# Kernel tuning notes

Hardware: AMD Instinct MI355X
Metric: run time of the kernel (lower is better)

## Reference

```python
import jax, jax.numpy as jnp
import numpy as np
from jax import lax

# Shared Conv2d [1,1] + BN + ReLU is represented as a per-point affine (BN folded
# into conv weight/bias at eval) followed by ReLU, matching inference-mode math.

B, N1, N2, K = 8, 8192, 2048, 8
C1, C2 = 64, 128
MLP0, MLP1, MLP2 = 128, 128, 128  # mlp=[128,128], mlp2=[128]


def setup_inputs() -> dict:
    key = jax.random.key(0)
    ks = jax.random.split(key, 10)
    sc = lambda fan_in: 1.0 / np.sqrt(fan_in)
    return {
        "xyz1": jax.random.normal(ks[0], (B, N1, 3), jnp.float32),
        "xyz2": jax.random.normal(ks[1], (B, N2, 3), jnp.float32),
        "feat1": jax.random.normal(ks[2], (B, N1, C1), jnp.float32),
        "feat2": jax.random.normal(ks[3], (B, N2, C2), jnp.float32),
        "W0": jax.random.normal(ks[4], (C2 + 3, MLP0), jnp.float32) * sc(C2 + 3),
        "b0": jnp.zeros((MLP0,), jnp.float32),
        "W1": jax.random.normal(ks[5], (MLP0, MLP1), jnp.float32) * sc(MLP0),
        "b1": jnp.zeros((MLP1,), jnp.float32),
        "W2": jax.random.normal(ks[6], (MLP1 + C1, MLP2), jnp.float32) * sc(MLP1 + C1),
        "b2": jnp.zeros((MLP2,), jnp.float32),
    }


def _knn_idx(xyz1, xyz2, k):
    # squared distances (B, N1, N2); top-k nearest in xyz2 for each xyz1 point
    d2 = jnp.sum((xyz1[:, :, None, :] - xyz2[:, None, :, :]) ** 2, axis=-1)
    _, idx = lax.top_k(-d2, k)  # (B, N1, K)
    return idx


def _gather(src, idx):
    # src: (B, N2, C), idx: (B, N1, K) -> (B, N1, K, C)
    return jax.vmap(lambda s, i: s[i])(src, idx)


def reference(xyz1, xyz2, feat1, feat2, W0, b0, W1, b1, W2, b2):
    idx = _knn_idx(xyz1, xyz2, K)
    xyz2_g = _gather(xyz2, idx)            # (B, N1, K, 3)
    feat2_g = _gather(feat2, idx)          # (B, N1, K, C2)
    xyz_diff = xyz2_g - xyz1[:, :, None, :]
    net = jnp.concatenate([feat2_g, xyz_diff], axis=-1)  # (B, N1, K, C2+3)
    net = jax.nn.relu(net @ W0 + b0)
    net = jax.nn.relu(net @ W1 + b1)       # (B, N1, K, MLP1)
    pooled = jnp.max(net, axis=2)          # max pooling over neighbors
    cat = jnp.concatenate([pooled, feat1], axis=-1)      # (B, N1, MLP1+C1)
    out = jax.nn.relu(cat @ W2 + b2)       # (B, N1, MLP2)
    return out
```

## Files before the change

kernel.cpp:

```cpp
#include <hip/hip_runtime.h>
#include <hip/hip_bf16.h>

constexpr int B_  = 8;
constexpr int N1_ = 8192;
constexpr int N2_ = 2048;
constexpr int K_  = 8;

typedef short bf16x8 __attribute__((ext_vector_type(8)));
typedef float f32x4  __attribute__((ext_vector_type(4)));

__device__ __forceinline__ short f2b(float x) {
    __hip_bfloat16 h = __float2bfloat16(x);
    return *reinterpret_cast<short*>(&h);
}

#define CASF(a, b) { const float _lo = fminf(a, b); \
                     const float _hi = fmaxf(a, b); \
                     (a) = _lo; (b) = _hi; }

__global__ __launch_bounds__(256) void prep_feat2(const float* __restrict__ feat2,
                                                  short* __restrict__ feat2b) {
    const int i = blockIdx.x * 256 + threadIdx.x;
    const float4 v = ((const float4*)feat2)[i];
    uint2 o;
    o.x = (unsigned short)f2b(v.x) | ((unsigned)(unsigned short)f2b(v.y) << 16);
    o.y = (unsigned short)f2b(v.z) | ((unsigned)(unsigned short)f2b(v.w) << 16);
    ((uint2*)feat2b)[i] = o;
}

__global__ __launch_bounds__(256) void prep_weights(
    const float* __restrict__ W0, const float* __restrict__ W1,
    const float* __restrict__ W2, const float* __restrict__ xyz2,
    short* __restrict__ W0T, short* __restrict__ W1T, short* __restrict__ W2T,
    float4* __restrict__ xpack) {
    int i = blockIdx.x * 256 + threadIdx.x;
    if (i < 128 * 160) {
        const int n = i / 160, k = i % 160;
        W0T[i] = (k < 131) ? f2b(W0[k * 128 + n]) : (short)0;
        return;
    }
    i -= 128 * 160;
    if (i < 128 * 128) {
        const int n = i >> 7, k = i & 127;
        W1T[i] = f2b(W1[k * 128 + n]);
        return;
    }
    i -= 128 * 128;
    if (i < 128 * 192) {
        const int n = i / 192, k = i % 192;
        W2T[i] = f2b(W2[k * 128 + n]);
        return;
    }
    i -= 128 * 192;
    xpack[i] = make_float4(xyz2[i * 3 + 0], xyz2[i * 3 + 1], xyz2[i * 3 + 2], 0.f);
}

constexpr int LCAP = 76;

__global__ __launch_bounds__(256) void knn_lazy(const float* __restrict__ xyz1,
                                                const float4* __restrict__ xpack,
                                                int* __restrict__ idx) {
    __shared__ __align__(16) unsigned short sMem[78 * 256];
    float* sD = (float*)sMem;
    int*   sI = (int*)sMem + 64 * 33;

    const int b = blockIdx.y;
    const int lane = threadIdx.x & 63;
    const int s = threadIdx.x >> 6;
    const int tid = threadIdx.x;
    const int n = blockIdx.x * 64 + lane;

    const float* q = xyz1 + ((size_t)b * N1_ + n) * 3;
    const float qx = q[0], qy = q[1], qz = q[2];
    const float4* P = xpack + (size_t)b * N2_ + s * 512;

    float bd[K_];
#pragma unroll
    for (int t = 0; t < K_; ++t) bd[t] = 3.0e38f;
    int cnt = 0;

    for (int j0 = 0; j0 < 512; j0 += 8) {
        float xf[8];
#pragma unroll
        for (int u = 0; u < 8; ++u) {
#pragma clang fp contract(off)
            const float4 p = P[j0 + u];
            const float dx = qx - p.x;
            const float dy = qy - p.y;
            const float dz = qz - p.z;
            const float dx2 = dx * dx;
            const float dy2 = dy * dy;
            const float dz2 = dz * dz;
            xf[u] = (dx2 + dy2) + dz2;
        }
        const float thr = bd[K_ - 1];
#pragma unroll
        for (int u = 0; u < 8; ++u) {
            const bool acc = xf[u] < thr;
            if (acc) {
                const int capped = cnt < LCAP ? cnt : LCAP;
                sMem[capped * 256 + tid] = (unsigned short)(j0 + u);
                cnt++;
            }
        }
        CASF(xf[0], xf[1]); CASF(xf[2], xf[3]); CASF(xf[4], xf[5]); CASF(xf[6], xf[7]);
        CASF(xf[0], xf[2]); CASF(xf[1], xf[3]); CASF(xf[4], xf[6]); CASF(xf[5], xf[7]);
        CASF(xf[1], xf[2]); CASF(xf[5], xf[6]); CASF(xf[0], xf[4]); CASF(xf[3], xf[7]);
        CASF(xf[1], xf[5]); CASF(xf[2], xf[6]);
        CASF(xf[1], xf[4]); CASF(xf[3], xf[6]);
        CASF(xf[2], xf[4]); CASF(xf[3], xf[5]);
        CASF(xf[3], xf[4]);
        float t0 = fminf(bd[0], xf[7]);
        float t1 = fminf(bd[1], xf[6]);
        float t2 = fminf(bd[2], xf[5]);
        float t3 = fminf(bd[3], xf[4]);
        float t4 = fminf(bd[4], xf[3]);
        float t5 = fminf(bd[5], xf[2]);
        float t6 = fminf(bd[6], xf[1]);
        float t7 = fminf(bd[7], xf[0]);
        CASF(t0, t4); CASF(t1, t5); CASF(t2, t6); CASF(t3, t7);
        CASF(t0, t2); CASF(t1, t3); CASF(t4, t6); CASF(t5, t7);
        CASF(t0, t1); CASF(t2, t3); CASF(t4, t5); CASF(t6, t7);
        bd[0] = t0; bd[1] = t1; bd[2] = t2; bd[3] = t3;
        bd[4] = t4; bd[5] = t5; bd[6] = t6; bd[7] = t7;
    }

    float rd[K_];
    int   ri[K_];
#pragma unroll
    for (int t = 0; t < K_; ++t) { rd[t] = 3.0e38f; ri[t] = 0; }
    const int m = cnt < LCAP ? cnt : LCAP;
    for (int t = 0;; ++t) {
        const bool act = t < m;
        if (!__any(act)) break;
        if (act) {
#pragma clang fp contract(off)
            const int jl = sMem[t * 256 + tid];
            const float4 p = P[jl];
            const float dx = qx - p.x;
            const float dy = qy - p.y;
            const float dz = qz - p.z;
            const float dx2 = dx * dx;
            const float dy2 = dy * dy;
            const float dz2 = dz * dz;
            const float d2 = (dx2 + dy2) + dz2;
            if (d2 < rd[K_ - 1]) {
                rd[K_ - 1] = d2; ri[K_ - 1] = s * 512 + jl;
#pragma unroll
                for (int t2 = K_ - 1; t2 >= 1; --t2) {
                    if (rd[t2] < rd[t2 - 1]) {
                        float td = rd[t2]; rd[t2] = rd[t2 - 1]; rd[t2 - 1] = td;
                        int   ti = ri[t2]; ri[t2] = ri[t2 - 1]; ri[t2 - 1] = ti;
                    }
                }
            }
        }
    }

    if (__any(cnt > LCAP)) {
        if (cnt > LCAP) {
#pragma unroll
            for (int t = 0; t < K_; ++t) { rd[t] = 3.0e38f; ri[t] = 0; }
            for (int j = 0; j < 512; ++j) {
#pragma clang fp contract(off)
                const float4 p = P[j];
                const float dx = qx - p.x;
                const float dy = qy - p.y;
                const float dz = qz - p.z;
                const float dx2 = dx * dx;
                const float dy2 = dy * dy;
                const float dz2 = dz * dz;
                const float d2 = (dx2 + dy2) + dz2;
                if (d2 < rd[K_ - 1]) {
                    rd[K_ - 1] = d2; ri[K_ - 1] = s * 512 + j;
#pragma unroll
                    for (int t2 = K_ - 1; t2 >= 1; --t2) {
                        if (rd[t2] < rd[t2 - 1]) {
                            float td = rd[t2]; rd[t2] = rd[t2 - 1]; rd[t2 - 1] = td;
                            int   ti = ri[t2]; ri[t2] = ri[t2 - 1]; ri[t2 - 1] = ti;
                        }
                    }
                }
            }
        }
    }

    __syncthreads();
#pragma unroll
    for (int t = 0; t < K_; ++t) {
        sD[lane * 33 + s * 8 + t] = rd[t];
        sI[lane * 33 + s * 8 + t] = ri[t];
    }
    __syncthreads();

    if (tid < 64) {
        const int qq = tid;
        int h[4] = {0, 0, 0, 0};
        const int base = (b * N1_ + n) * K_;
#pragma unroll
        for (int t = 0; t < K_; ++t) {
            float best = 3.1e38f;
            int   bidx = 0, bs = 0;
#pragma unroll
            for (int ss = 0; ss < 4; ++ss) {
                if (h[ss] < 8) {
                    const float d = sD[qq * 33 + ss * 8 + h[ss]];
                    if (d < best) { best = d; bidx = sI[qq * 33 + ss * 8 + h[ss]]; bs = ss; }
                }
            }
#pragma unroll
            for (int ss = 0; ss < 4; ++ss) h[ss] += (ss == bs) ? 1 : 0;
            idx[base + t] = bidx;
        }
    }
}

__global__ __launch_bounds__(256) void fused_mfma(
    const float* __restrict__ xyz1, const float* __restrict__ xyz2,
    const float* __restrict__ feat1,
    const float* __restrict__ b0, const float* __restrict__ b1,
    const float* __restrict__ b2,
    const short* __restrict__ feat2b, const short* __restrict__ W0T,
    const short* __restrict__ W1T, const short* __restrict__ W2T,
    const int* __restrict__ idx, float* __restrict__ out) {
    __shared__ __align__(16) short sA[128 * 168];
    __shared__ __align__(16) short sCat[16 * 200];

    const int b = blockIdx.y;
    const int n0 = blockIdx.x * 16;
    const int tid = threadIdx.x;

    {
        const int row = tid >> 1, half = tid & 1;
        const int p = row >> 3, kk = row & 7;
        const int n = n0 + p;
        const int j = idx[((size_t)b * N1_ + n) * K_ + kk];
        const uint4* src = (const uint4*)(feat2b + ((size_t)(b * N2_ + j)) * 128 + half * 64);
        uint4* dst = (uint4*)(sA + row * 168 + half * 64);
#pragma unroll
        for (int t = 0; t < 8; ++t) dst[t] = src[t];
        uint4* pad = (uint4*)(sA + row * 168 + 128 + half * 16);
        if (half == 0) {
            const float dx = xyz2[((size_t)b * N2_ + j) * 3 + 0] - xyz1[((size_t)b * N1_ + n) * 3 + 0];
            const float dy = xyz2[((size_t)b * N2_ + j) * 3 + 1] - xyz1[((size_t)b * N1_ + n) * 3 + 1];
            const float dz = xyz2[((size_t)b * N2_ + j) * 3 + 2] - xyz1[((size_t)b * N1_ + n) * 3 + 2];
            uint4 v;
            v.x = (unsigned short)f2b(dx) | ((unsigned)(unsigned short)f2b(dy) << 16);
            v.y = (unsigned short)f2b(dz);
            v.z = 0; v.w = 0;
            pad[0] = v;
            pad[1] = make_uint4(0, 0, 0, 0);
        } else {
            pad[0] = make_uint4(0, 0, 0, 0);
            pad[1] = make_uint4(0, 0, 0, 0);
        }
    }
    {
#pragma unroll
        for (int u = 0; u < 4; ++u) {
            const int e = tid * 4 + u;
            const int p = e >> 6, c = e & 63;
            sCat[p * 200 + 128 + c] = f2b(feat1[((size_t)b * N1_ + n0 + p) * 64 + c]);
        }
    }
    __syncthreads();

    const int wave = tid >> 6, lane = tid & 63;
    const int q = lane >> 4, l15 = lane & 15;
    const int mBase = (wave & 1) * 64, nBase = (wave >> 1) * 64;

    const f32x4 zero4 = {0.f, 0.f, 0.f, 0.f};

    f32x4 acc[4][4];
#pragma unroll
    for (int mt = 0; mt < 4; ++mt)
#pragma unroll
        for (int nt = 0; nt < 4; ++nt) acc[mt][nt] = zero4;

    for (int ks = 0; ks < 5; ++ks) {
        bf16x8 af[4], bf[4];
#pragma unroll
        for (int mt = 0; mt < 4; ++mt)
            af[mt] = *(const bf16x8*)(sA + (mBase + mt * 16 + l15) * 168 + ks * 32 + q * 8);
#pragma unroll
        for (int nt = 0; nt < 4; ++nt)
            bf[nt] = *(const bf16x8*)(W0T + (nBase + nt * 16 + l15) * 160 + ks * 32 + q * 8);
#pragma unroll
        for (int mt = 0; mt < 4; ++mt)
#pragma unroll
            for (int nt = 0; nt < 4; ++nt)
                acc[mt][nt] = __builtin_amdgcn_mfma_f32_16x16x32_bf16(af[mt], bf[nt], acc[mt][nt], 0, 0, 0);
    }

    float b0v[4];
#pragma unroll
    for (int nt = 0; nt < 4; ++nt) b0v[nt] = b0[nBase + nt * 16 + l15];
    __syncthreads();
#pragma unroll
    for (int mt = 0; mt < 4; ++mt)
#pragma unroll
        for (int nt = 0; nt < 4; ++nt)
#pragma unroll
            for (int r = 0; r < 4; ++r) {
                const int row = mBase + mt * 16 + q * 4 + r;
                const int col = nBase + nt * 16 + l15;
                sA[row * 136 + col] = f2b(fmaxf(acc[mt][nt][r] + b0v[nt], 0.0f));
            }
    __syncthreads();

    f32x4 acc2[4][4];
#pragma unroll
    for (int mt = 0; mt < 4; ++mt)
#pragma unroll
        for (int nt = 0; nt < 4; ++nt) acc2[mt][nt] = zero4;

    for (int ks = 0; ks < 4; ++ks) {
        bf16x8 af[4], bf[4];
#pragma unroll
        for (int mt = 0; mt < 4; ++mt)
            af[mt] = *(const bf16x8*)(sA + (mBase + mt * 16 + l15) * 136 + ks * 32 + q * 8);
#pragma unroll
        for (int nt = 0; nt < 4; ++nt)
            bf[nt] = *(const bf16x8*)(W1T + (nBase + nt * 16 + l15) * 128 + ks * 32 + q * 8);
#pragma unroll
        for (int mt = 0; mt < 4; ++mt)
#pragma unroll
            for (int nt = 0; nt < 4; ++nt)
                acc2[mt][nt] = __builtin_amdgcn_mfma_f32_16x16x32_bf16(af[mt], bf[nt], acc2[mt][nt], 0, 0, 0);
    }

    float b1v[4];
#pragma unroll
    for (int nt = 0; nt < 4; ++nt) b1v[nt] = b1[nBase + nt * 16 + l15];
#pragma unroll
    for (int mt = 0; mt < 4; ++mt)
#pragma unroll
        for (int nt = 0; nt < 4; ++nt) {
            float vm = fmaxf(acc2[mt][nt][0] + b1v[nt], 0.0f);
#pragma unroll
            for (int r = 1; r < 4; ++r) vm = fmaxf(vm, acc2[mt][nt][r] + b1v[nt]);
            const float other = __shfl_xor(vm, 16);
            const float pool = fmaxf(vm, other);
            if ((q & 1) == 0) {
                const int pp = (mBase >> 3) + mt * 2 + (q >> 1);
                sCat[pp * 200 + nBase + nt * 16 + l15] = f2b(pool);
            }
        }
    __syncthreads();

    f32x4 acc3[2];
    acc3[0] = zero4; acc3[1] = zero4;
    const int nB2 = wave * 32;
    for (int ks = 0; ks < 6; ++ks) {
        const bf16x8 a2 = *(const bf16x8*)(sCat + l15 * 200 + ks * 32 + q * 8);
#pragma unroll
        for (int nt = 0; nt < 2; ++nt) {
            const bf16x8 b2f = *(const bf16x8*)(W2T + (nB2 + nt * 16 + l15) * 192 + ks * 32 + q * 8);
            acc3[nt] = __builtin_amdgcn_mfma_f32_16x16x32_bf16(a2, b2f, acc3[nt], 0, 0, 0);
        }
    }
    float b2v[2];
#pragma unroll
    for (int nt = 0; nt < 2; ++nt) b2v[nt] = b2[nB2 + nt * 16 + l15];
#pragma unroll
    for (int nt = 0; nt < 2; ++nt)
#pragma unroll
        for (int r = 0; r < 4; ++r) {
            const int p = q * 4 + r;
            const int col = nB2 + nt * 16 + l15;
            out[((size_t)(b * N1_ + n0 + p)) * 128 + col] = fmaxf(acc3[nt][r] + b2v[nt], 0.0f);
        }
}

extern "C" void kernel_launch(void* const* d_in, const int* in_sizes, int n_in,
                              void* d_out, int out_size, void* d_ws, size_t ws_size,
                              hipStream_t stream) {
    const float* xyz1  = (const float*)d_in[0];
    const float* xyz2  = (const float*)d_in[1];
    const float* feat1 = (const float*)d_in[2];
    const float* feat2 = (const float*)d_in[3];
    const float* W0    = (const float*)d_in[4];
    const float* b0    = (const float*)d_in[5];
    const float* W1    = (const float*)d_in[6];
    const float* b1    = (const float*)d_in[7];
    const float* W2    = (const float*)d_in[8];
    const float* b2    = (const float*)d_in[9];
    float* out = (float*)d_out;

    char* ws = (char*)d_ws;
    int*    idx    = (int*)(ws + 0);
    short*  feat2b = (short*)(ws + 2097152);
    short*  W0T    = (short*)(ws + 6291456);
    short*  W1T    = (short*)(ws + 6332416);
    short*  W2T    = (short*)(ws + 6365184);
    float4* xpack  = (float4*)(ws + 6414336);

    prep_feat2<<<2048, 256, 0, stream>>>(feat2, feat2b);
    prep_weights<<<304, 256, 0, stream>>>(W0, W1, W2, xyz2, W0T, W1T, W2T, xpack);
    knn_lazy<<<dim3(N1_ / 64, B_), 256, 0, stream>>>(xyz1, xpack, idx);
    fused_mfma<<<dim3(N1_ / 16, B_), 256, 0, stream>>>(xyz1, xyz2, feat1, b0, b1, b2,
                                                       feat2b, W0T, W1T, W2T, idx, out);
}
```

Baseline: 313.8 us.

## Use SoA xyz2 layout with packed f32x2 distance math and merge prep kernels

Stores xyz2 as separate x/y/z planes so the KNN candidate scan reads them with wide float4 loads. Distances are computed two at a time with packed 2-wide float vectors, and FMA contraction is now allowed there. The candidate threshold is widened slightly so that rounding differences from contraction cannot drop true neighbours; the exact rescoring pass still uses uncontracted math. The two prep kernels are merged into one launch to save launch overhead, at the cost of a slightly larger candidate list.

```diff
diff --git a/kernel.cpp b/kernel.cpp
--- a/kernel.cpp
+++ b/kernel.cpp
@@ -8,6 +8,7 @@
 
 typedef short bf16x8 __attribute__((ext_vector_type(8)));
 typedef float f32x4  __attribute__((ext_vector_type(4)));
+typedef float f32x2  __attribute__((ext_vector_type(2)));
 
 __device__ __forceinline__ short f2b(float x) {
     __hip_bfloat16 h = __float2bfloat16(x);
@@ -18,22 +19,22 @@
                      const float _hi = fmaxf(a, b); \
                      (a) = _lo; (b) = _hi; }
 
-__global__ __launch_bounds__(256) void prep_feat2(const float* __restrict__ feat2,
-                                                  short* __restrict__ feat2b) {
-    const int i = blockIdx.x * 256 + threadIdx.x;
-    const float4 v = ((const float4*)feat2)[i];
-    uint2 o;
-    o.x = (unsigned short)f2b(v.x) | ((unsigned)(unsigned short)f2b(v.y) << 16);
-    o.y = (unsigned short)f2b(v.z) | ((unsigned)(unsigned short)f2b(v.w) << 16);
-    ((uint2*)feat2b)[i] = o;
-}
-
-__global__ __launch_bounds__(256) void prep_weights(
+__global__ __launch_bounds__(256) void prep_all(
+    const float* __restrict__ feat2, short* __restrict__ feat2b,
     const float* __restrict__ W0, const float* __restrict__ W1,
     const float* __restrict__ W2, const float* __restrict__ xyz2,
     short* __restrict__ W0T, short* __restrict__ W1T, short* __restrict__ W2T,
-    float4* __restrict__ xpack) {
-    int i = blockIdx.x * 256 + threadIdx.x;
+    float* __restrict__ xp) {
+    if (blockIdx.x < 2048) {
+        const int i = blockIdx.x * 256 + threadIdx.x;
+        const float4 v = ((const float4*)feat2)[i];
+        uint2 o;
+        o.x = (unsigned short)f2b(v.x) | ((unsigned)(unsigned short)f2b(v.y) << 16);
+        o.y = (unsigned short)f2b(v.z) | ((unsigned)(unsigned short)f2b(v.w) << 16);
+        ((uint2*)feat2b)[i] = o;
+        return;
+    }
+    int i = (blockIdx.x - 2048) * 256 + threadIdx.x;
     if (i < 128 * 160) {
         const int n = i / 160, k = i % 160;
         W0T[i] = (k < 131) ? f2b(W0[k * 128 + n]) : (short)0;
@@ -52,13 +53,18 @@
         return;
     }
     i -= 128 * 192;
-    xpack[i] = make_float4(xyz2[i * 3 + 0], xyz2[i * 3 + 1], xyz2[i * 3 + 2], 0.f);
+    const int b = i >> 11, j = i & 2047;
+    const float* src = xyz2 + ((size_t)b * N2_ + j) * 3;
+    float* dst = xp + (size_t)b * 3 * N2_ + j;
+    dst[0]        = src[0];
+    dst[N2_]      = src[1];
+    dst[2 * N2_]  = src[2];
 }
 
 constexpr int LCAP = 76;
 
 __global__ __launch_bounds__(256) void knn_lazy(const float* __restrict__ xyz1,
-                                                const float4* __restrict__ xpack,
+                                                const float* __restrict__ xp,
                                                 int* __restrict__ idx) {
     __shared__ __align__(16) unsigned short sMem[78 * 256];
     float* sD = (float*)sMem;
@@ -72,28 +78,37 @@
 
     const float* q = xyz1 + ((size_t)b * N1_ + n) * 3;
     const float qx = q[0], qy = q[1], qz = q[2];
-    const float4* P = xpack + (size_t)b * N2_ + s * 512;
+    const float* xs = xp + (size_t)b * 3 * N2_ + s * 512;
+    const float* ys = xs + N2_;
+    const float* zs = xs + 2 * N2_;
 
     float bd[K_];
 #pragma unroll
     for (int t = 0; t < K_; ++t) bd[t] = 3.0e38f;
     int cnt = 0;
 
+    const f32x2 qx2 = {qx, qx}, qy2 = {qy, qy}, qz2 = {qz, qz};
+
     for (int j0 = 0; j0 < 512; j0 += 8) {
+        const float4 X0 = *(const float4*)(xs + j0);
+        const float4 X1 = *(const float4*)(xs + j0 + 4);
+        const float4 Y0 = *(const float4*)(ys + j0);
+        const float4 Y1 = *(const float4*)(ys + j0 + 4);
+        const float4 Z0 = *(const float4*)(zs + j0);
+        const float4 Z1 = *(const float4*)(zs + j0 + 4);
         float xf[8];
-#pragma unroll
-        for (int u = 0; u < 8; ++u) {
-#pragma clang fp contract(off)
-            const float4 p = P[j0 + u];
-            const float dx = qx - p.x;
-            const float dy = qy - p.y;
-            const float dz = qz - p.z;
-            const float dx2 = dx * dx;
-            const float dy2 = dy * dy;
-            const float dz2 = dz * dz;
-            xf[u] = (dx2 + dy2) + dz2;
-        }
-        const float thr = bd[K_ - 1];
+        {
+            f32x2 dx, dy, dz, d;
+            dx = qx2 - f32x2{X0.x, X0.y}; dy = qy2 - f32x2{Y0.x, Y0.y}; dz = qz2 - f32x2{Z0.x, Z0.y};
+            d = dx * dx + dy * dy + dz * dz; xf[0] = d.x; xf[1] = d.y;
+            dx = qx2 - f32x2{X0.z, X0.w}; dy = qy2 - f32x2{Y0.z, Y0.w}; dz = qz2 - f32x2{Z0.z, Z0.w};
+            d = dx * dx + dy * dy + dz * dz; xf[2] = d.x; xf[3] = d.y;
+            dx = qx2 - f32x2{X1.x, X1.y}; dy = qy2 - f32x2{Y1.x, Y1.y}; dz = qz2 - f32x2{Z1.x, Z1.y};
+            d = dx * dx + dy * dy + dz * dz; xf[4] = d.x; xf[5] = d.y;
+            dx = qx2 - f32x2{X1.z, X1.w}; dy = qy2 - f32x2{Y1.z, Y1.w}; dz = qz2 - f32x2{Z1.z, Z1.w};
+            d = dx * dx + dy * dy + dz * dz; xf[6] = d.x; xf[7] = d.y;
+        }
+        const float thr = bd[K_ - 1] * 1.0000038f;
 #pragma unroll
         for (int u = 0; u < 8; ++u) {
             const bool acc = xf[u] < thr;
@@ -136,10 +151,9 @@
         if (act) {
 #pragma clang fp contract(off)
             const int jl = sMem[t * 256 + tid];
-            const float4 p = P[jl];
-            const float dx = qx - p.x;
-            const float dy = qy - p.y;
-            const float dz = qz - p.z;
+            const float dx = qx - xs[jl];
+            const float dy = qy - ys[jl];
+            const float dz = qz - zs[jl];
             const float dx2 = dx * dx;
             const float dy2 = dy * dy;
             const float dz2 = dz * dz;
@@ -163,10 +177,9 @@
             for (int t = 0; t < K_; ++t) { rd[t] = 3.0e38f; ri[t] = 0; }
             for (int j = 0; j < 512; ++j) {
 #pragma clang fp contract(off)
-                const float4 p = P[j];
-                const float dx = qx - p.x;
-                const float dy = qy - p.y;
-                const float dz = qz - p.z;
+                const float dx = qx - xs[j];
+                const float dy = qy - ys[j];
+                const float dz = qz - zs[j];
                 const float dx2 = dx * dx;
                 const float dy2 = dy * dy;
                 const float dz2 = dz * dz;
@@ -393,11 +406,11 @@
     short*  W0T    = (short*)(ws + 6291456);
     short*  W1T    = (short*)(ws + 6332416);
     short*  W2T    = (short*)(ws + 6365184);
-    float4* xpack  = (float4*)(ws + 6414336);
-
-    prep_feat2<<<2048, 256, 0, stream>>>(feat2, feat2b);
-    prep_weights<<<304, 256, 0, stream>>>(W0, W1, W2, xyz2, W0T, W1T, W2T, xpack);
-    knn_lazy<<<dim3(N1_ / 64, B_), 256, 0, stream>>>(xyz1, xpack, idx);
+    float*  xp     = (float*)(ws + 6414336);
+
+    prep_all<<<2352, 256, 0, stream>>>(feat2, feat2b, W0, W1, W2, xyz2,
+                                       W0T, W1T, W2T, xp);
+    knn_lazy<<<dim3(N1_ / 64, B_), 256, 0, stream>>>(xyz1, xp, idx);
     fused_mfma<<<dim3(N1_ / 16, B_), 256, 0, stream>>>(xyz1, xyz2, feat1, b0, b1, b2,
                                                        feat2b, W0T, W1T, W2T, idx, out);
 }
```

After: 315.5 us. Within noise of the previous version (+0.5%).
